# Kernel optimization log

Measured on AMD Instinct MI355X. Metric: run time of the kernel, lower is better.

## Reference

```python
import jax, jax.numpy as jnp
import numpy as np

B, A, UNITS, HID, T = 16, 256, 64, 64, 3


def setup_inputs() -> dict:
    key = jax.random.key(0)
    ks = jax.random.split(key, 16)
    x = jax.random.normal(ks[0], (B, A + 2, A), dtype=jnp.float32)
    # GNN message-passing weights (torch.randn in original)
    W0 = jax.random.normal(ks[1], (1, UNITS), dtype=jnp.float32)
    W1 = jax.random.normal(ks[2], (UNITS, UNITS), dtype=jnp.float32)
    W2 = jax.random.normal(ks[3], (UNITS, UNITS), dtype=jnp.float32)
    W3 = jax.random.normal(ks[4], (1, UNITS), dtype=jnp.float32)
    # fc_a: Linear(64,64)->ReLU->Linear(64,32)->ReLU->Linear(32,1); stored (in,out)
    s = lambda k, i, o: jax.random.uniform(k, (i, o), jnp.float32, -1, 1) / np.sqrt(i)
    sb = lambda k, i, o: jax.random.uniform(k, (o,), jnp.float32, -1, 1) / np.sqrt(i)
    a_w1, a_b1 = s(ks[5], UNITS, HID), sb(ks[6], UNITS, HID)
    a_w2, a_b2 = s(ks[7], HID, HID // 2), sb(ks[8], HID, HID // 2)
    a_w3, a_b3 = s(ks[9], HID // 2, 1), sb(ks[10], HID // 2, 1)
    # fc_v: Linear(64,64)->ReLU->Linear(64,1)
    v_w1, v_b1 = s(ks[11], UNITS, HID), sb(ks[12], UNITS, HID)
    v_w2, v_b2 = s(ks[13], HID, 1), sb(ks[14], HID, 1)
    return dict(x=x, W0=W0, W1=W1, W2=W2, W3=W3,
                a_w1=a_w1, a_b1=a_b1, a_w2=a_w2, a_b2=a_b2, a_w3=a_w3, a_b3=a_b3,
                v_w1=v_w1, v_b1=v_b1, v_w2=v_w2, v_b2=v_b2)


def reference(x, W0, W1, W2, W3,
              a_w1, a_b1, a_w2, a_b2, a_w3, a_b3,
              v_w1, v_b1, v_w2, v_b2):
    n_actions = x.shape[2]                       # A
    cur_sol = x[:, 0, :][..., None]              # [B, A, 1]
    mask = x[:, 1, :]                            # [B, A]
    weights = x[:, 2:n_actions + 2, :]           # [B, A, A]
    adjacent = (weights != 0).astype(jnp.float32)
    embedding = jnp.zeros((x.shape[0], n_actions, UNITS), dtype=jnp.float32)

    # e3 is loop-invariant in math, but original recomputes each step; keep T small python loop (faithful, T=3 static)
    for _ in range(T):
        e1 = cur_sol @ W0                                        # [B,A,1]@[1,U] -> [B,A,U]
        e2 = (adjacent @ embedding / n_actions) @ W1             # [B,A,U]
        # weights.reshape(B,A,A,1) @ W3(1,U) == outer-product broadcast
        e3_ = jnp.sum(jax.nn.relu(weights[..., None] * W3[0]), axis=2) / n_actions  # [B,A,U]
        e3 = e3_ @ W2
        embedding = jax.nn.relu(e1 + e2 + e3)

    # dueling heads
    h = jax.nn.relu(embedding @ a_w1 + a_b1)
    h = jax.nn.relu(h @ a_w2 + a_b2)
    out_a = (h @ a_w3 + a_b3)[..., 0]                            # [B, A]
    hv = jax.nn.relu(embedding @ v_w1 + v_b1)
    out_v = (hv @ v_w2 + v_b2)[..., 0]                           # [B, A]
    out_v = jnp.sum(out_v, axis=1, keepdims=True)                # [B, 1]
    output = out_v + (out_a - jnp.sum(out_a, axis=1, keepdims=True))
    output = output + mask * 10.0                                # hard_mask=False
    return output
```

## Files before the change

### kernel.cpp

```cpp
#include <hip/hip_runtime.h>


#define MC  0x5F3A9C71u
#define MD  0x5F3A9C72u
#define MDN 0x5F3A9C73u

__device__ __forceinline__ float reluf(float v) { return fmaxf(v, 0.f); }

__global__ __launch_bounds__(256) void k_fused(
    const float* __restrict__ x,
    const float* __restrict__ W0, const float* __restrict__ W1,
    const float* __restrict__ W2, const float* __restrict__ W3,
    const float* __restrict__ aw1, const float* __restrict__ ab1,
    const float* __restrict__ aw2, const float* __restrict__ ab2,
    const float* __restrict__ aw3, const float* __restrict__ ab3,
    const float* __restrict__ vw1, const float* __restrict__ vb1,
    const float* __restrict__ vw2, const float* __restrict__ vb2,
    unsigned long long* __restrict__ statsg,
    float* __restrict__ partA, float* __restrict__ partV,
    unsigned int* __restrict__ flagg, unsigned int* __restrict__ flag2,
    float* __restrict__ embg, float* __restrict__ out)
{
    __shared__ float aw1s[4096], vw1s[4096], W1s[4096];
    __shared__ float aw2s[64 * 36];
    __shared__ float embsT[64 * 36];
    __shared__ float poss[256], negs[256], css[256];
    __shared__ float W0s[64], P2s[64], N2s[64], Ssh[64], e2c[64];
    __shared__ float wpart[256], npart[256];
    __shared__ float ab1s[64], vb1s[64], vw2s[64], ab2s[32], aw3s[32];
    __shared__ float ab3s[1], vb2s[1], sov[32], soa[32];
    __shared__ float pstash[8], qstash[8];
    __shared__ int zw[4];
    __shared__ unsigned int sflags[8];
    __shared__ int zrow[256];
    __shared__ unsigned long long zmsL[1024];

    const float invA = 1.0f / 256.0f;
    const int t = threadIdx.x;
    const int batch = blockIdx.x & 15;
    const int sub   = blockIdx.x >> 4;
    const int obase = sub * 32;

    css[t] = x[(size_t)batch * 66048 + t];
    float maskv = 0.f;
    if (t < 32) maskv = x[((size_t)batch * 258 + 1) * 256 + obase + t];

    {
        int r8 = t >> 3, s8 = t & 7;
        int grow = obase + r8;
        const float* rowp = x + ((size_t)batch * 258 + 2 + grow) * 256 + s8 * 32;
        float pp = 0.f, nn = 0.f, mn = 1e30f;
        #pragma unroll
        for (int c = 0; c < 32; c += 4) {
            float4 v = *(const float4*)(rowp + c);
            pp += fmaxf(v.x, 0.f) + fmaxf(v.y, 0.f) + fmaxf(v.z, 0.f) + fmaxf(v.w, 0.f);
            nn += fminf(v.x, 0.f) + fminf(v.y, 0.f) + fminf(v.z, 0.f) + fminf(v.w, 0.f);
            mn = fminf(mn, fminf(fminf(fabsf(v.x), fabsf(v.y)),
                                 fminf(fabsf(v.z), fabsf(v.w))));
        }
        pp += __shfl_xor(pp, 1); pp += __shfl_xor(pp, 2); pp += __shfl_xor(pp, 4);
        nn += __shfl_xor(nn, 1); nn += __shfl_xor(nn, 2); nn += __shfl_xor(nn, 4);
        mn = fminf(mn, __shfl_xor(mn, 1));
        mn = fminf(mn, __shfl_xor(mn, 2));
        mn = fminf(mn, __shfl_xor(mn, 4));
        if (s8 == 0) {
            float2 f2 = make_float2(pp, nn);
            unsigned long long pk;
            __builtin_memcpy(&pk, &f2, 8);
            __hip_atomic_store(&statsg[batch * 256 + grow], pk,
                               __ATOMIC_RELAXED, __HIP_MEMORY_SCOPE_AGENT);
        }
        int z = (s8 == 0 && mn == 0.f) ? 1 : 0;
        unsigned long long b = __ballot(z);
        if ((t & 63) == 0) zw[t >> 6] = (b != 0ull);
    }
    __syncthreads();
    if (t == 0) {
        unsigned int fv = (zw[0] | zw[1] | zw[2] | zw[3]) ? MD : MC;
        __hip_atomic_store(&flagg[blockIdx.x], fv,
                           __ATOMIC_RELEASE, __HIP_MEMORY_SCOPE_AGENT);
    }

    {
        int j = t & 63, mg = t >> 6;
        float pa = 0.f, na = 0.f;
        #pragma unroll
        for (int k = 0; k < 16; ++k) {
            int m = mg * 16 + k;
            float w3 = W3[m];
            float w2 = W2[m * 64 + j];
            pa = fmaf(fmaxf(w3, 0.f), w2, pa);
            na = fmaf(fminf(w3, 0.f), w2, na);
        }
        wpart[mg * 64 + j] = pa;
        npart[mg * 64 + j] = na;
    }
    #pragma unroll
    for (int k = 0; k < 4; ++k) {
        int idx = k * 1024 + t * 4;
        *(float4*)&aw1s[idx] = *(const float4*)&aw1[idx];
        *(float4*)&vw1s[idx] = *(const float4*)&vw1[idx];
        *(float4*)&W1s[idx]  = *(const float4*)&W1[idx];
    }
    #pragma unroll
    for (int k = 0; k < 8; ++k) {
        int idx = k * 256 + t;
        aw2s[(idx >> 5) * 36 + (idx & 31)] = aw2[idx];
    }
    if (t < 64) { W0s[t] = W0[t]; ab1s[t] = ab1[t]; vb1s[t] = vb1[t]; vw2s[t] = vw2[t]; }
    if (t >= 64 && t < 96) { ab2s[t - 64] = ab2[t - 64]; aw3s[t - 64] = aw3[t - 64]; }
    if (t == 96) { ab3s[0] = ab3[0]; vb2s[0] = vb2[0]; }
    __syncthreads();
    if (t < 64) {
        P2s[t] = wpart[t] + wpart[64 + t] + wpart[128 + t] + wpart[192 + t];
        N2s[t] = npart[t] + npart[64 + t] + npart[128 + t] + npart[192 + t];
    }
    if (t < 8) {
        const unsigned int* f = &flagg[t * 16 + batch];
        unsigned int v = __hip_atomic_load(f, __ATOMIC_ACQUIRE, __HIP_MEMORY_SCOPE_AGENT);
        while (v != MC && v != MD) {
            __builtin_amdgcn_s_sleep(1);
            v = __hip_atomic_load(f, __ATOMIC_ACQUIRE, __HIP_MEMORY_SCOPE_AGENT);
        }
        sflags[t] = v;
    }
    __syncthreads();
    const int dirty = (sflags[0] == MD) | (sflags[1] == MD) | (sflags[2] == MD) |
                      (sflags[3] == MD) | (sflags[4] == MD) | (sflags[5] == MD) |
                      (sflags[6] == MD) | (sflags[7] == MD);

    {
        unsigned long long pk = __hip_atomic_load(&statsg[batch * 256 + t],
                                 __ATOMIC_RELAXED, __HIP_MEMORY_SCOPE_AGENT);
        float2 f2;
        __builtin_memcpy(&f2, &pk, 8);
        poss[t] = f2.x;
        negs[t] = f2.y;
    }
    __syncthreads();

    if (!dirty) {
        const int j = t & 63, rg = t >> 6;
        const float w0j = W0s[j], p2j = P2s[j], n2j = N2s[j];
        float c_j = 0.f;
        #pragma unroll
        for (int iter = 0; iter < 2; ++iter) {
            float s = 0.f;
            #pragma unroll 8
            for (int k = 0; k < 64; ++k) {
                int i = rg * 64 + k;
                s += reluf(fmaf(css[i], w0j, (poss[i] * p2j + negs[i] * n2j) * invA) + c_j);
            }
            wpart[rg * 64 + j] = s;
            __syncthreads();
            if (t < 64) {
                float S = wpart[t] + wpart[64 + t] + wpart[128 + t] + wpart[192 + t];
                Ssh[t] = S;
                float c = 0.f;
                #pragma unroll 8
                for (int m = 0; m < 64; ++m) c = fmaf(Ssh[m], W1s[m * 64 + t], c);
                e2c[t] = c * invA;
            }
            __syncthreads();
            c_j = e2c[j];
        }
        {
            int r = t & 31, mg = t >> 5;
            int grow = obase + r;
            float cs = css[grow], pi = poss[grow], ni = negs[grow];
            #pragma unroll
            for (int jj = 0; jj < 8; ++jj) {
                int m = mg * 8 + jj;
                embsT[m * 36 + r] = reluf(fmaf(cs, W0s[m],
                                    (pi * P2s[m] + ni * N2s[m]) * invA) + e2c[m]);
            }
        }
    } else {
        {
            const int r4 = t >> 2, sub4 = t & 3;
            #pragma unroll
            for (int p = 0; p < 4; ++p) {
                int row = p * 64 + r4;
                const float* rowp = x + ((size_t)batch * 258 + 2 + row) * 256 + sub4 * 64;
                unsigned long long zm = 0ull;
                for (int c = 0; c < 64; ++c)
                    if (rowp[c] == 0.f) zm |= 1ull << c;
                zmsL[row * 4 + sub4] = zm;
                int zf = (zm != 0ull);
                zf |= __shfl_xor(zf, 1); zf |= __shfl_xor(zf, 2);
                if (sub4 == 0) zrow[row] = zf;
            }
        }
        __syncthreads();
        float* eb0 = embg + (size_t)blockIdx.x * 32768;
        float* eb1 = eb0 + 16384;
        const int r4 = t >> 2, sub4 = t & 3, jb = sub4 * 16;
        #pragma unroll
        for (int p = 0; p < 4; ++p) {
            int row = p * 64 + r4;
            float cs = css[row], pi = poss[row], ni = negs[row];
            #pragma unroll
            for (int q = 0; q < 16; ++q) {
                int jj = jb + q;
                eb0[row * 64 + jj] = reluf(fmaf(cs, W0s[jj],
                                      (pi * P2s[jj] + ni * N2s[jj]) * invA));
            }
        }
        __syncthreads();
        float* cur = eb0; float* nxt = eb1;
        for (int it = 1; it <= 2; ++it) {
            {
                int j = t & 63, rg = t >> 6;
                float s = 0.f;
                for (int k = 0; k < 64; ++k) s += cur[(rg * 64 + k) * 64 + j];
                wpart[rg * 64 + j] = s;
            }
            __syncthreads();
            if (t < 64) {
                float S = wpart[t] + wpart[64 + t] + wpart[128 + t] + wpart[192 + t];
                Ssh[t] = S;
                float c = 0.f;
                for (int m = 0; m < 64; ++m) c = fmaf(Ssh[m], W1s[m * 64 + t], c);
                e2c[t] = c * invA;
            }
            __syncthreads();
            #pragma unroll
            for (int p = 0; p < 4; ++p) {
                int row = p * 64 + r4;
                float cs = css[row], pi = poss[row], ni = negs[row];
                float acc[16];
                #pragma unroll
                for (int q = 0; q < 16; ++q) {
                    int jj = jb + q;
                    acc[q] = fmaf(cs, W0s[jj], (pi * P2s[jj] + ni * N2s[jj]) * invA)
                             + e2c[jj];
                }
                if (zrow[row]) {
                    for (int wd = 0; wd < 4; ++wd) {
                        unsigned long long zm = zmsL[row * 4 + wd];
                        while (zm) {
                            int k = wd * 64 + __builtin_ctzll(zm);
                            zm &= zm - 1;
                            float corr[16];
                            #pragma unroll
                            for (int q = 0; q < 16; ++q) corr[q] = 0.f;
                            for (int m = 0; m < 64; ++m) {
                                float ebm = cur[k * 64 + m];
                                #pragma unroll
                                for (int q = 0; q < 16; ++q)
                                    corr[q] = fmaf(ebm, W1s[m * 64 + jb + q], corr[q]);
                            }
                            #pragma unroll
                            for (int q = 0; q < 16; ++q) acc[q] -= corr[q] * invA;
                        }
                    }
                }
                #pragma unroll
                for (int q = 0; q < 16; ++q)
                    nxt[row * 64 + jb + q] = reluf(acc[q]);
            }
            __syncthreads();
            float* tmp = cur; cur = nxt; nxt = tmp;
        }
        for (int idx = t; idx < 2048; idx += 256) {
            int r = idx & 31, m = idx >> 5;
            embsT[m * 36 + r] = cur[(obase + r) * 64 + m];
        }
    }
    __syncthreads();

    const int cg  = t & 31;
    const int rg4 = t >> 5;
    float aA0x = 0.f, aA0y = 0.f, aA1x = 0.f, aA1y = 0.f;
    float aA2x = 0.f, aA2y = 0.f, aA3x = 0.f, aA3y = 0.f;
    float aV0x = 0.f, aV0y = 0.f, aV1x = 0.f, aV1y = 0.f;
    float aV2x = 0.f, aV2y = 0.f, aV3x = 0.f, aV3y = 0.f;
    for (int m = 0; m < 64; ++m) {
        float4 em = *(const float4*)&embsT[m * 36 + rg4 * 4];
        float2 a2 = *(const float2*)&aw1s[m * 64 + 2 * cg];
        float2 v2 = *(const float2*)&vw1s[m * 64 + 2 * cg];
        aA0x = fmaf(em.x, a2.x, aA0x); aA0y = fmaf(em.x, a2.y, aA0y);
        aA1x = fmaf(em.y, a2.x, aA1x); aA1y = fmaf(em.y, a2.y, aA1y);
        aA2x = fmaf(em.z, a2.x, aA2x); aA2y = fmaf(em.z, a2.y, aA2y);
        aA3x = fmaf(em.w, a2.x, aA3x); aA3y = fmaf(em.w, a2.y, aA3y);
        aV0x = fmaf(em.x, v2.x, aV0x); aV0y = fmaf(em.x, v2.y, aV0y);
        aV1x = fmaf(em.y, v2.x, aV1x); aV1y = fmaf(em.y, v2.y, aV1y);
        aV2x = fmaf(em.z, v2.x, aV2x); aV2y = fmaf(em.z, v2.y, aV2y);
        aV3x = fmaf(em.w, v2.x, aV3x); aV3y = fmaf(em.w, v2.y, aV3y);
    }
    float wvx = vw2s[2 * cg], wvy = vw2s[2 * cg + 1];
    float pv0 = fmaf(reluf(aV0x + vb1s[2 * cg]), wvx, reluf(aV0y + vb1s[2 * cg + 1]) * wvy);
    float pv1 = fmaf(reluf(aV1x + vb1s[2 * cg]), wvx, reluf(aV1y + vb1s[2 * cg + 1]) * wvy);
    float pv2 = fmaf(reluf(aV2x + vb1s[2 * cg]), wvx, reluf(aV2y + vb1s[2 * cg + 1]) * wvy);
    float pv3 = fmaf(reluf(aV3x + vb1s[2 * cg]), wvx, reluf(aV3y + vb1s[2 * cg + 1]) * wvy);
    #pragma unroll
    for (int mk = 1; mk <= 16; mk <<= 1) {
        pv0 += __shfl_xor(pv0, mk); pv1 += __shfl_xor(pv1, mk);
        pv2 += __shfl_xor(pv2, mk); pv3 += __shfl_xor(pv3, mk);
    }
    float b0 = ab1s[2 * cg], b1 = ab1s[2 * cg + 1];
    float h00 = reluf(aA0x + b0), h01 = reluf(aA0y + b1);
    float h10 = reluf(aA1x + b0), h11 = reluf(aA1y + b1);
    float h20 = reluf(aA2x + b0), h21 = reluf(aA2y + b1);
    float h30 = reluf(aA3x + b0), h31 = reluf(aA3y + b1);
    __syncthreads();
    float* h1s = embsT;
    *(float2*)&h1s[(rg4 * 4 + 0) * 66 + 2 * cg] = make_float2(h00, h01);
    *(float2*)&h1s[(rg4 * 4 + 1) * 66 + 2 * cg] = make_float2(h10, h11);
    *(float2*)&h1s[(rg4 * 4 + 2) * 66 + 2 * cg] = make_float2(h20, h21);
    *(float2*)&h1s[(rg4 * 4 + 3) * 66 + 2 * cg] = make_float2(h30, h31);
    if (cg == 0) {
        sov[rg4 * 4 + 0] = pv0 + vb2s[0];
        sov[rg4 * 4 + 1] = pv1 + vb2s[0];
        sov[rg4 * 4 + 2] = pv2 + vb2s[0];
        sov[rg4 * 4 + 3] = pv3 + vb2s[0];
    }
    __syncthreads();

    {
        int r = t >> 3, jg = t & 7;
        float c0 = 0.f, c1 = 0.f, c2 = 0.f, c3 = 0.f;
        for (int q = 0; q < 64; ++q) {
            float h = h1s[r * 66 + q];
            float4 w = *(const float4*)&aw2s[q * 36 + jg * 4];
            c0 = fmaf(h, w.x, c0); c1 = fmaf(h, w.y, c1);
            c2 = fmaf(h, w.z, c2); c3 = fmaf(h, w.w, c3);
        }
        float part = reluf(c0 + ab2s[jg * 4 + 0]) * aw3s[jg * 4 + 0];
        part = fmaf(reluf(c1 + ab2s[jg * 4 + 1]), aw3s[jg * 4 + 1], part);
        part = fmaf(reluf(c2 + ab2s[jg * 4 + 2]), aw3s[jg * 4 + 2], part);
        part = fmaf(reluf(c3 + ab2s[jg * 4 + 3]), aw3s[jg * 4 + 3], part);
        part += __shfl_xor(part, 1);
        part += __shfl_xor(part, 2);
        part += __shfl_xor(part, 4);
        if (jg == 0) soa[r] = part + ab3s[0];
    }
    __syncthreads();

    if (t < 32) {
        float a = soa[t], v = sov[t];
        #pragma unroll
        for (int mk = 1; mk <= 16; mk <<= 1) {
            a += __shfl_xor(a, mk);
            v += __shfl_xor(v, mk);
        }
        if (t == 0) {
            __hip_atomic_store(&partA[blockIdx.x], a,
                               __ATOMIC_RELAXED, __HIP_MEMORY_SCOPE_AGENT);
            __hip_atomic_store(&partV[blockIdx.x], v,
                               __ATOMIC_RELAXED, __HIP_MEMORY_SCOPE_AGENT);
            __hip_atomic_store(&flag2[blockIdx.x], MDN,
                               __ATOMIC_RELEASE, __HIP_MEMORY_SCOPE_AGENT);
        }
    }
    if (t < 8) {
        const unsigned int* f = &flag2[t * 16 + batch];
        unsigned int v = __hip_atomic_load(f, __ATOMIC_ACQUIRE, __HIP_MEMORY_SCOPE_AGENT);
        while (v != MDN) {
            __builtin_amdgcn_s_sleep(1);
            v = __hip_atomic_load(f, __ATOMIC_ACQUIRE, __HIP_MEMORY_SCOPE_AGENT);
        }
        pstash[t] = __hip_atomic_load(&partA[t * 16 + batch],
                                      __ATOMIC_RELAXED, __HIP_MEMORY_SCOPE_AGENT);
        qstash[t] = __hip_atomic_load(&partV[t * 16 + batch],
                                      __ATOMIC_RELAXED, __HIP_MEMORY_SCOPE_AGENT);
    }
    __syncthreads();

    if (t < 32) {
        float sA = pstash[0];
        sA += pstash[1]; sA += pstash[2]; sA += pstash[3];
        sA += pstash[4]; sA += pstash[5]; sA += pstash[6]; sA += pstash[7];
        float sV = qstash[0];
        sV += qstash[1]; sV += qstash[2]; sV += qstash[3];
        sV += qstash[4]; sV += qstash[5]; sV += qstash[6]; sV += qstash[7];
        out[batch * 256 + obase + t] = sV + soa[t] - sA + maskv * 10.0f;
    }
}

extern "C" void kernel_launch(void* const* d_in, const int* in_sizes, int n_in,
                              void* d_out, int out_size, void* d_ws, size_t ws_size,
                              hipStream_t stream)
{
    (void)in_sizes; (void)n_in; (void)out_size; (void)ws_size;
    const float* x   = (const float*)d_in[0];
    const float* W0  = (const float*)d_in[1];
    const float* W1  = (const float*)d_in[2];
    const float* W2  = (const float*)d_in[3];
    const float* W3  = (const float*)d_in[4];
    const float* aw1 = (const float*)d_in[5];
    const float* ab1 = (const float*)d_in[6];
    const float* aw2 = (const float*)d_in[7];
    const float* ab2 = (const float*)d_in[8];
    const float* aw3 = (const float*)d_in[9];
    const float* ab3 = (const float*)d_in[10];
    const float* vw1 = (const float*)d_in[11];
    const float* vb1 = (const float*)d_in[12];
    const float* vw2 = (const float*)d_in[13];
    const float* vb2 = (const float*)d_in[14];

    float* ws = (float*)d_ws;
    unsigned long long* statsg = (unsigned long long*)ws;
    float* partA = ws + 8192;
    float* partV = ws + 8320;
    unsigned int* flagg = (unsigned int*)(ws + 8448);
    unsigned int* flag2 = (unsigned int*)(ws + 8576);
    float* embg  = ws + 16384;

    k_fused<<<128, 256, 0, stream>>>(x, W0, W1, W2, W3,
                                     aw1, ab1, aw2, ab2, aw3, ab3,
                                     vw1, vb1, vw2, vb2,
                                     statsg, partA, partV, flagg, flag2,
                                     embg, (float*)d_out);
}
```

Measured before the change: 24.80 us.

## Compute full-batch row stats per block instead of cross-block flag exchange

Before, the 8 blocks sharing a batch each reduced 32 rows of the weight matrix, published per-row positive/negative sums and a zero flag to global memory, then spin-waited on each other's flags. Now every block reads all 256 rows of its batch itself and writes the sums straight to shared memory, which removes the global atomics and the inter-block spin barrier. Separately, the aw1 and vw1 weights are interleaved into one shared array so the head GEMM needs a single float4 LDS load per step. The price is 8x redundant reading of each batch's 256x256 matrix, mostly hitting in L2.

```diff
diff --git a/kernel.cpp b/kernel.cpp
--- a/kernel.cpp
+++ b/kernel.cpp
@@ -1,8 +1,6 @@
 #include <hip/hip_runtime.h>
 
 
-#define MC  0x5F3A9C71u
-#define MD  0x5F3A9C72u
 #define MDN 0x5F3A9C73u
 
 __device__ __forceinline__ float reluf(float v) { return fmaxf(v, 0.f); }
@@ -16,12 +14,12 @@
     const float* __restrict__ aw3, const float* __restrict__ ab3,
     const float* __restrict__ vw1, const float* __restrict__ vb1,
     const float* __restrict__ vw2, const float* __restrict__ vb2,
-    unsigned long long* __restrict__ statsg,
     float* __restrict__ partA, float* __restrict__ partV,
-    unsigned int* __restrict__ flagg, unsigned int* __restrict__ flag2,
+    unsigned int* __restrict__ flag2,
     float* __restrict__ embg, float* __restrict__ out)
 {
-    __shared__ float aw1s[4096], vw1s[4096], W1s[4096];
+    __shared__ float awvs[2048 * 4];
+    __shared__ float W1s[4096];
     __shared__ float aw2s[64 * 36];
     __shared__ float embsT[64 * 36];
     __shared__ float poss[256], negs[256], css[256];
@@ -31,7 +29,6 @@
     __shared__ float ab3s[1], vb2s[1], sov[32], soa[32];
     __shared__ float pstash[8], qstash[8];
     __shared__ int zw[4];
-    __shared__ unsigned int sflags[8];
     __shared__ int zrow[256];
     __shared__ unsigned long long zmsL[1024];
 
@@ -45,40 +42,29 @@
     float maskv = 0.f;
     if (t < 32) maskv = x[((size_t)batch * 258 + 1) * 256 + obase + t];
 
+    int zacc = 0;
     {
-        int r8 = t >> 3, s8 = t & 7;
-        int grow = obase + r8;
-        const float* rowp = x + ((size_t)batch * 258 + 2 + grow) * 256 + s8 * 32;
-        float pp = 0.f, nn = 0.f, mn = 1e30f;
-        #pragma unroll
-        for (int c = 0; c < 32; c += 4) {
-            float4 v = *(const float4*)(rowp + c);
-            pp += fmaxf(v.x, 0.f) + fmaxf(v.y, 0.f) + fmaxf(v.z, 0.f) + fmaxf(v.w, 0.f);
-            nn += fminf(v.x, 0.f) + fminf(v.y, 0.f) + fminf(v.z, 0.f) + fminf(v.w, 0.f);
-            mn = fminf(mn, fminf(fminf(fabsf(v.x), fabsf(v.y)),
-                                 fminf(fabsf(v.z), fabsf(v.w))));
-        }
-        pp += __shfl_xor(pp, 1); pp += __shfl_xor(pp, 2); pp += __shfl_xor(pp, 4);
-        nn += __shfl_xor(nn, 1); nn += __shfl_xor(nn, 2); nn += __shfl_xor(nn, 4);
-        mn = fminf(mn, __shfl_xor(mn, 1));
-        mn = fminf(mn, __shfl_xor(mn, 2));
-        mn = fminf(mn, __shfl_xor(mn, 4));
-        if (s8 == 0) {
-            float2 f2 = make_float2(pp, nn);
-            unsigned long long pk;
-            __builtin_memcpy(&pk, &f2, 8);
-            __hip_atomic_store(&statsg[batch * 256 + grow], pk,
-                               __ATOMIC_RELAXED, __HIP_MEMORY_SCOPE_AGENT);
-        }
-        int z = (s8 == 0 && mn == 0.f) ? 1 : 0;
-        unsigned long long b = __ballot(z);
+        const int r4 = t >> 2, sub4 = t & 3;
+        #pragma unroll
+        for (int p = 0; p < 4; ++p) {
+            int row = p * 64 + r4;
+            const float* rowp = x + ((size_t)batch * 258 + 2 + row) * 256 + sub4 * 64;
+            float pp = 0.f, nn = 0.f;
+            int zf = 0;
+            #pragma unroll
+            for (int c = 0; c < 64; c += 4) {
+                float4 v = *(const float4*)(rowp + c);
+                pp += fmaxf(v.x, 0.f) + fmaxf(v.y, 0.f) + fmaxf(v.z, 0.f) + fmaxf(v.w, 0.f);
+                nn += fminf(v.x, 0.f) + fminf(v.y, 0.f) + fminf(v.z, 0.f) + fminf(v.w, 0.f);
+                zf |= (v.x == 0.f) | (v.y == 0.f) | (v.z == 0.f) | (v.w == 0.f);
+            }
+            pp += __shfl_xor(pp, 1); pp += __shfl_xor(pp, 2);
+            nn += __shfl_xor(nn, 1); nn += __shfl_xor(nn, 2);
+            if (sub4 == 0) { poss[row] = pp; negs[row] = nn; }
+            zacc |= zf;
+        }
+        unsigned long long b = __ballot(zacc != 0);
         if ((t & 63) == 0) zw[t >> 6] = (b != 0ull);
-    }
-    __syncthreads();
-    if (t == 0) {
-        unsigned int fv = (zw[0] | zw[1] | zw[2] | zw[3]) ? MD : MC;
-        __hip_atomic_store(&flagg[blockIdx.x], fv,
-                           __ATOMIC_RELEASE, __HIP_MEMORY_SCOPE_AGENT);
     }
 
     {
@@ -98,9 +84,15 @@
     #pragma unroll
     for (int k = 0; k < 4; ++k) {
         int idx = k * 1024 + t * 4;
-        *(float4*)&aw1s[idx] = *(const float4*)&aw1[idx];
-        *(float4*)&vw1s[idx] = *(const float4*)&vw1[idx];
-        *(float4*)&W1s[idx]  = *(const float4*)&W1[idx];
+        *(float4*)&W1s[idx] = *(const float4*)&W1[idx];
+    }
+    #pragma unroll
+    for (int k = 0; k < 8; ++k) {
+        int e = k * 256 + t;
+        int m = e >> 5, cgi = e & 31;
+        float2 a = *(const float2*)&aw1[m * 64 + 2 * cgi];
+        float2 v = *(const float2*)&vw1[m * 64 + 2 * cgi];
+        *(float4*)&awvs[e * 4] = make_float4(a.x, a.y, v.x, v.y);
     }
     #pragma unroll
     for (int k = 0; k < 8; ++k) {
@@ -115,29 +107,8 @@
         P2s[t] = wpart[t] + wpart[64 + t] + wpart[128 + t] + wpart[192 + t];
         N2s[t] = npart[t] + npart[64 + t] + npart[128 + t] + npart[192 + t];
     }
-    if (t < 8) {
-        const unsigned int* f = &flagg[t * 16 + batch];
-        unsigned int v = __hip_atomic_load(f, __ATOMIC_ACQUIRE, __HIP_MEMORY_SCOPE_AGENT);
-        while (v != MC && v != MD) {
-            __builtin_amdgcn_s_sleep(1);
-            v = __hip_atomic_load(f, __ATOMIC_ACQUIRE, __HIP_MEMORY_SCOPE_AGENT);
-        }
-        sflags[t] = v;
-    }
-    __syncthreads();
-    const int dirty = (sflags[0] == MD) | (sflags[1] == MD) | (sflags[2] == MD) |
-                      (sflags[3] == MD) | (sflags[4] == MD) | (sflags[5] == MD) |
-                      (sflags[6] == MD) | (sflags[7] == MD);
-
-    {
-        unsigned long long pk = __hip_atomic_load(&statsg[batch * 256 + t],
-                                 __ATOMIC_RELAXED, __HIP_MEMORY_SCOPE_AGENT);
-        float2 f2;
-        __builtin_memcpy(&f2, &pk, 8);
-        poss[t] = f2.x;
-        negs[t] = f2.y;
-    }
-    __syncthreads();
+    __syncthreads();
+    const int dirty = zw[0] | zw[1] | zw[2] | zw[3];
 
     if (!dirty) {
         const int j = t & 63, rg = t >> 6;
@@ -277,16 +248,15 @@
     float aV2x = 0.f, aV2y = 0.f, aV3x = 0.f, aV3y = 0.f;
     for (int m = 0; m < 64; ++m) {
         float4 em = *(const float4*)&embsT[m * 36 + rg4 * 4];
-        float2 a2 = *(const float2*)&aw1s[m * 64 + 2 * cg];
-        float2 v2 = *(const float2*)&vw1s[m * 64 + 2 * cg];
-        aA0x = fmaf(em.x, a2.x, aA0x); aA0y = fmaf(em.x, a2.y, aA0y);
-        aA1x = fmaf(em.y, a2.x, aA1x); aA1y = fmaf(em.y, a2.y, aA1y);
-        aA2x = fmaf(em.z, a2.x, aA2x); aA2y = fmaf(em.z, a2.y, aA2y);
-        aA3x = fmaf(em.w, a2.x, aA3x); aA3y = fmaf(em.w, a2.y, aA3y);
-        aV0x = fmaf(em.x, v2.x, aV0x); aV0y = fmaf(em.x, v2.y, aV0y);
-        aV1x = fmaf(em.y, v2.x, aV1x); aV1y = fmaf(em.y, v2.y, aV1y);
-        aV2x = fmaf(em.z, v2.x, aV2x); aV2y = fmaf(em.z, v2.y, aV2y);
-        aV3x = fmaf(em.w, v2.x, aV3x); aV3y = fmaf(em.w, v2.y, aV3y);
+        float4 w  = *(const float4*)&awvs[(m * 32 + cg) * 4];
+        aA0x = fmaf(em.x, w.x, aA0x); aA0y = fmaf(em.x, w.y, aA0y);
+        aA1x = fmaf(em.y, w.x, aA1x); aA1y = fmaf(em.y, w.y, aA1y);
+        aA2x = fmaf(em.z, w.x, aA2x); aA2y = fmaf(em.z, w.y, aA2y);
+        aA3x = fmaf(em.w, w.x, aA3x); aA3y = fmaf(em.w, w.y, aA3y);
+        aV0x = fmaf(em.x, w.z, aV0x); aV0y = fmaf(em.x, w.w, aV0y);
+        aV1x = fmaf(em.y, w.z, aV1x); aV1y = fmaf(em.y, w.w, aV1y);
+        aV2x = fmaf(em.z, w.z, aV2x); aV2y = fmaf(em.z, w.w, aV2y);
+        aV3x = fmaf(em.w, w.z, aV3x); aV3y = fmaf(em.w, w.w, aV3y);
     }
     float wvx = vw2s[2 * cg], wvy = vw2s[2 * cg + 1];
     float pv0 = fmaf(reluf(aV0x + vb1s[2 * cg]), wvx, reluf(aV0y + vb1s[2 * cg + 1]) * wvy);
@@ -400,16 +370,14 @@
     const float* vb2 = (const float*)d_in[14];
 
     float* ws = (float*)d_ws;
-    unsigned long long* statsg = (unsigned long long*)ws;
-    float* partA = ws + 8192;
-    float* partV = ws + 8320;
-    unsigned int* flagg = (unsigned int*)(ws + 8448);
-    unsigned int* flag2 = (unsigned int*)(ws + 8576);
-    float* embg  = ws + 16384;
+    float* partA = ws;
+    float* partV = ws + 128;
+    unsigned int* flag2 = (unsigned int*)(ws + 256);
+    float* embg  = ws + 1024;
 
     k_fused<<<128, 256, 0, stream>>>(x, W0, W1, W2, W3,
                                      aw1, ab1, aw2, ab2, aw3, ab3,
                                      vw1, vb1, vw2, vb2,
-                                     statsg, partA, partV, flagg, flag2,
+                                     partA, partV, flag2,
                                      embg, (float*)d_out);
 }
```

Result: slower. 30.81 us (+24.2%).
